# Performance work log

Hardware: AMD Instinct MI355X
Metric: run time of the kernel (lower is better)

Reference implementation:

```python
import jax, jax.numpy as jnp
import numpy as np

BN_EPS = 1e-5


def setup_inputs() -> dict:
    key = jax.random.key(0)
    ks = jax.random.split(key, 5)
    B, T, N, C, O, K, E = 2, 4, 50000, 32, 32, 3, 800000
    x = jax.random.normal(ks[0], (B, T, N, C), dtype=jnp.float32)
    edge_index = jax.random.randint(ks[1], (2, E), 0, N, dtype=jnp.int64)
    edge_weight = jax.random.uniform(ks[2], (E,), dtype=jnp.float32)
    W = jax.random.normal(ks[3], (K, C, O), dtype=jnp.float32) * 0.05
    bias = jnp.zeros((O,), dtype=jnp.float32)
    gamma = jnp.ones((O,), dtype=jnp.float32)
    beta = jnp.zeros((O,), dtype=jnp.float32)
    return {"x": x, "edge_index": edge_index, "edge_weight": edge_weight,
            "W": W, "bias": bias, "gamma": gamma, "beta": beta}


def reference(x, edge_index, edge_weight, W, bias, gamma, beta):
    # x: [B, T, N, C]; edge_index: [2, E]; W: [K, C, O]
    B, T, N, C = x.shape
    K = W.shape[0]
    src, dst = edge_index[0], edge_index[1]

    # Scaled Laplacian L_hat = 2L/lambda_max - I with sym norm, lambda_max=2
    # => L_hat = -D^{-1/2} A D^{-1/2} (zero diagonal), PyG ChebConv default.
    deg = jax.ops.segment_sum(edge_weight, src, num_segments=N)
    safe = jnp.where(deg > 0, deg, 1.0)
    dinv = jnp.where(deg > 0, 1.0 / jnp.sqrt(safe), 0.0)
    norm = -dinv[src] * edge_weight * dinv[dst]  # [E]

    # Batch all (b, t) slices together: [N, M, C] with M = B*T
    xn = jnp.transpose(x, (2, 0, 1, 3)).reshape(N, B * T, C)

    def lap(z):  # sparse SpMM applied to every (b,t) slice at once
        return jax.ops.segment_sum(norm[:, None, None] * z[src], dst,
                                   num_segments=N)

    # Chebyshev recursion: T0 = x, T1 = L_hat x, Tk = 2 L_hat T_{k-1} - T_{k-2}
    Tx_prev2 = xn
    out = jnp.einsum('nmc,co->nmo', Tx_prev2, W[0])
    if K > 1:
        Tx_prev = lap(xn)
        out = out + jnp.einsum('nmc,co->nmo', Tx_prev, W[1])
        for k in range(2, K):
            Tx_k = 2.0 * lap(Tx_prev) - Tx_prev2
            out = out + jnp.einsum('nmc,co->nmo', Tx_k, W[k])
            Tx_prev2, Tx_prev = Tx_prev, Tx_k
    out = out + bias  # [N, M, O]

    # BatchNorm1d in training mode, applied per (b,t) slice over nodes,
    # exactly as the original per-slice loop does (biased variance).
    mean = jnp.mean(out, axis=0, keepdims=True)              # [1, M, O]
    var = jnp.mean((out - mean) ** 2, axis=0, keepdims=True)  # [1, M, O]
    y = gamma * (out - mean) * jax.lax.rsqrt(var + BN_EPS) + beta
    y = jax.nn.relu(y)

    return jnp.transpose(y.reshape(N, B, T, -1), (1, 2, 0, 3))  # [B,T,N,O]
```

## Files before the change

### kernel.cpp

```cpp
#include <hip/hip_runtime.h>

#define NNODES 50000
#define NEDGES 800000
#define MB 8
#define CF 32
#define OF 32
#define FPN 256
#define TOTAL_OUT (MB * NNODES * OF)
#define NREP 8

#define BSH 9
#define BINW 512
#define NB ((NNODES + BINW - 1) / BINW)
#define PH (NB * 2)
#define NBA 512
#define EPB ((NEDGES + NBA - 1) / NBA)
#define CAPL 30
#define LBW 32
#define CH 16
#define BINCAP 14336
#define STCAP 7168
#define WFB ((NNODES / 16 + 3) / 4)
#define DGRID ((NNODES + 1023) / 1024)

typedef unsigned short ushort_t;
typedef unsigned int uint_t;
typedef __attribute__((ext_vector_type(8))) short bf16x8;
typedef __attribute__((ext_vector_type(4))) float f32x4;

__device__ __forceinline__ ushort_t f2bf(float f) {
    uint_t u = __float_as_uint(f);
    u += 0x7FFFu + ((u >> 16) & 1u);
    return (ushort_t)(u >> 16);
}
__device__ __forceinline__ float bflo(uint_t u) { return __uint_as_float(u << 16); }
__device__ __forceinline__ float bfhi(uint_t u) { return __uint_as_float(u & 0xFFFF0000u); }

__device__ __forceinline__ bool detect_is64(const int* ei) {
    int lane = threadIdx.x & 63;
    int v = ei[2 * lane + 1];
    return __ballot(v != 0) == 0ULL;
}

__global__ void __launch_bounds__(256) k_build(const int* __restrict__ ei,
                                               const float* __restrict__ w,
                                               const float* __restrict__ x,
                                               float* __restrict__ deg8,
                                               int* __restrict__ g_cnt,
                                               int* __restrict__ g_realH,
                                               int2* __restrict__ binD,
                                               ushort_t* __restrict__ xn) {
    int blk = blockIdx.x;
    int t = threadIdx.x;
    __shared__ int l_cnt[NB];
    __shared__ int l_base[NB];
    __shared__ ushort_t l_pfx[NB + 1];
    __shared__ int l_half[PH];
    __shared__ int2 l_buf[NB][LBW];
    if (blk < NBA) {
        bool is64 = detect_is64(ei);
        const int2* ei2 = (const int2*)ei;
        for (int i = t; i < NB; i += 256) l_cnt[i] = 0;
        for (int i = t; i < PH; i += 256) l_half[i] = 0;
        __syncthreads();
        int rep = blk & 7;
        int e0 = blk * EPB;
        int e1 = min(e0 + EPB, NEDGES);
        for (int e = e0 + t; e < e1; e += 256) {
            int s, d;
            if (is64) {
                int2 sv = ei2[e];
                int2 dv = ei2[NEDGES + e];
                s = sv.x; d = dv.x;
            } else {
                s = ei[e]; d = ei[NEDGES + e];
            }
            float wt = w[e];
            atomicAdd(&deg8[(size_t)rep * NNODES + s], wt);
            int bin = d >> BSH;
            int half = (d >> 8) & 1;
            int2 entry;
            entry.x = s | ((d & (BINW - 1)) << 16);
            entry.y = __float_as_int(wt);
            int pos = atomicAdd(&l_cnt[bin], 1);
            if (pos < CAPL) {
                l_buf[bin][pos] = entry;
                atomicAdd(&l_half[bin * 2 + half], 1);
            } else {
                int gp = atomicAdd(&g_cnt[bin], 1);
                if (gp < BINCAP) {
                    binD[(size_t)bin * BINCAP + gp] = entry;
                    atomicAdd(&g_realH[bin * 2 + half], 1);
                }
            }
        }
        __syncthreads();
        if (t < NB) {
            int c = min(l_cnt[t], CAPL);
            int p = (c + CH - 1) & ~(CH - 1);
            for (int i = c; i < p; i++) l_buf[t][i] = make_int2(0, 0);
            l_cnt[t] = p;
            if (p > 0) l_base[t] = atomicAdd(&g_cnt[t], p);
        }
        for (int i = t; i < PH; i += 256)
            if (l_half[i] > 0) atomicAdd(&g_realH[i], l_half[i]);
        __syncthreads();
        if (t == 0) {
            int sacc = 0;
            for (int b2 = 0; b2 < NB; b2++) {
                l_pfx[b2] = (ushort_t)sacc;
                sacc += l_cnt[b2];
            }
            l_pfx[NB] = (ushort_t)sacc;
        }
        __syncthreads();
        int total = l_pfx[NB];
        for (int idx = t; idx < total; idx += 256) {
            int lo = 0, hi = NB - 1;
            while (lo < hi) {
                int mid = (lo + hi + 1) >> 1;
                if ((int)l_pfx[mid] <= idx) lo = mid; else hi = mid - 1;
            }
            int rel = idx - (int)l_pfx[lo];
            int gp = l_base[lo] + rel;
            if (gp < BINCAP) binD[(size_t)lo * BINCAP + gp] = l_buf[lo][rel];
        }
    } else {
        int bb = blk - NBA;
        int lane = t & 63;
        int n = bb * 4 + (t >> 6);
        int m = lane >> 3;
        int c = (4 * lane) & 31;
        const float4 v = *(const float4*)(x + ((size_t)m * NNODES + n) * CF + c);
        uint2 d;
        d.x = (uint_t)f2bf(v.x) | ((uint_t)f2bf(v.y) << 16);
        d.y = (uint_t)f2bf(v.z) | ((uint_t)f2bf(v.w) << 16);
        *(uint2*)(xn + (size_t)n * FPN + 4 * lane) = d;
    }
}

__global__ void __launch_bounds__(256) k_pass2(const int* __restrict__ g_cnt,
                                               const int* __restrict__ g_realH,
                                               const int2* __restrict__ binD,
                                               const float* __restrict__ deg8,
                                               int2* __restrict__ csr,
                                               int* __restrict__ csr_off,
                                               float* __restrict__ dinv) {
    __shared__ int2 l_stage[STCAP];
    __shared__ int l_h[256];
    __shared__ int l_ws[4];
    __shared__ int l_red[4];
    __shared__ int l_tot;
    int b = blockIdx.x;
    int t = threadIdx.x;
    if (b >= PH) {
        int n = (b - PH) * 1024 + t;
        #pragma unroll
        for (int i = 0; i < 4; i++, n += 256) {
            if (n < NNODES) {
                float s = 0.0f;
                #pragma unroll
                for (int r = 0; r < NREP; r++) s += deg8[(size_t)r * NNODES + n];
                dinv[n] = (s > 0.0f) ? (1.0f / sqrtf(s)) : 0.0f;
            }
        }
        return;
    }
    int bin = b >> 1, h = b & 1;
    int lane = t & 63, wv = t >> 6;

    int vb = (t < b) ? g_realH[t] : 0;
    #pragma unroll
    for (int off = 32; off >= 1; off >>= 1) vb += __shfl_down(vb, off);
    if (lane == 0) l_red[wv] = vb;
    l_h[t] = 0;
    __syncthreads();
    int base = l_red[0] + l_red[1] + l_red[2] + l_red[3];

    int cnt = min(g_cnt[bin], BINCAP);
    const int2* bp = binD + (size_t)bin * BINCAP;
    for (int i = t; i < cnt; i += 256) {
        int2 e = bp[i];
        int dl = e.x >> 16;
        if (e.y != 0 && (dl >> 8) == h) atomicAdd(&l_h[dl & 255], 1);
    }
    __syncthreads();

    int a0 = l_h[t];
    int v = a0;
    #pragma unroll
    for (int off = 1; off < 64; off <<= 1) {
        int u = __shfl_up(v, off);
        if (lane >= off) v += u;
    }
    if (lane == 63) l_ws[wv] = v;
    __syncthreads();
    int wpre = 0;
    for (int i = 0; i < wv; i++) wpre += l_ws[i];
    int excl = wpre + v - a0;

    int n = bin * BINW + h * 256 + t;
    if (n < NNODES) csr_off[n] = base + excl;
    l_h[t] = excl;
    if (t == 255) {
        l_tot = excl + a0;
        if (b == PH - 1) csr_off[NNODES] = base + excl + a0;
    }
    __syncthreads();

    for (int i = t; i < cnt; i += 256) {
        int2 e = bp[i];
        int dl = e.x >> 16;
        if (e.y != 0 && (dl >> 8) == h) {
            int slot = atomicAdd(&l_h[dl & 255], 1);
            if (slot < STCAP) l_stage[slot] = make_int2(e.x & 0xFFFF, e.y);
        }
    }
    __syncthreads();

    int tot = min(l_tot, STCAP);
    for (int i = t; i < tot; i += 256) csr[(size_t)base + i] = l_stage[i];
}

template <int PHASE>
__global__ void __launch_bounds__(256) k_spmm(const ushort_t* __restrict__ src,
                                              const ushort_t* __restrict__ xn0,
                                              const int* __restrict__ csr_off,
                                              const int2* __restrict__ csr,
                                              const float* __restrict__ dinv,
                                              ushort_t* __restrict__ dst) {
    int t = threadIdx.x;
    int lane = t & 63;
    int n = __builtin_amdgcn_readfirstlane(blockIdx.x * 4 + (t >> 6));
    int off = csr_off[n];
    int cnt = min(csr_off[n + 1] - off, 64);
    float dn = dinv[n];
    float a0 = 0.0f, a1 = 0.0f, a2 = 0.0f, a3 = 0.0f;
    if (cnt > 0) {
        int j = off + min(lane, cnt - 1);
        int2 ed = csr[j];
        int cv = ed.x;
        float vw = -dinv[cv] * __int_as_float(ed.y) * dn;
        uint_t vv = __float_as_uint(vw);
        for (int k = 0; k < cnt; k += 16) {
            int sc[16]; float v[16];
            #pragma unroll
            for (int i = 0; i < 16; i++) {
                sc[i] = __builtin_amdgcn_readlane(cv, k + i);
                float vr = __uint_as_float(__builtin_amdgcn_readlane((int)vv, k + i));
                v[i] = (k + i < cnt) ? vr : 0.0f;
            }
            uint2 u[16];
            #pragma unroll
            for (int i = 0; i < 16; i++)
                u[i] = *(const uint2*)(src + (size_t)sc[i] * FPN + 4 * lane);
            #pragma unroll
            for (int i = 0; i < 16; i++) {
                a0 += v[i] * bflo(u[i].x);
                a1 += v[i] * bfhi(u[i].x);
                a2 += v[i] * bflo(u[i].y);
                a3 += v[i] * bfhi(u[i].y);
            }
        }
    }
    if (PHASE == 2) {
        const uint2 xu = *(const uint2*)(xn0 + (size_t)n * FPN + 4 * lane);
        a0 = 2.0f * a0 - bflo(xu.x);
        a1 = 2.0f * a1 - bfhi(xu.x);
        a2 = 2.0f * a2 - bflo(xu.y);
        a3 = 2.0f * a3 - bfhi(xu.y);
    }
    uint2 d;
    d.x = (uint_t)f2bf(a0) | ((uint_t)f2bf(a1) << 16);
    d.y = (uint_t)f2bf(a2) | ((uint_t)f2bf(a3) << 16);
    *(uint2*)(dst + (size_t)n * FPN + 4 * lane) = d;
}

__global__ void k_wprep(const float* __restrict__ W, ushort_t* __restrict__ wbf) {
    int tid = threadIdx.x;
    for (int i = tid; i < 384; i += 256) {
        int k    = i >> 7;
        int rem  = i & 127;
        int oh   = rem >> 6;
        int lane = rem & 63;
        int quad = lane >> 4;
        int colc = lane & 15;
        ushort_t* d = wbf + (size_t)i * 8;
        for (int j = 0; j < 8; j++) {
            int c = quad * 8 + j;
            int o = oh * 16 + colc;
            d[j] = f2bf(W[k * (CF * OF) + c * OF + o]);
        }
    }
}

__global__ void __launch_bounds__(256) k_wfuse(const ushort_t* __restrict__ xn,
                                               const ushort_t* __restrict__ t1,
                                               const ushort_t* __restrict__ t2,
                                               const ushort_t* __restrict__ wbf,
                                               const float* __restrict__ bias,
                                               float* __restrict__ out) {
    int t = threadIdx.x;
    int lane = t & 63;
    int wv = blockIdx.x * 4 + (t >> 6);
    if (wv >= NNODES / 16) return;
    int n0 = wv * 16;
    int quad = lane >> 4, col = lane & 15;

    bf16x8 B[6];
    #pragma unroll
    for (int i = 0; i < 6; i++)
        B[i] = *(const bf16x8*)(wbf + (size_t)(i * 64 + lane) * 8);
    float blo = bias[col], bhi = bias[16 + col];

    size_t aoff = (size_t)(n0 + col) * FPN + quad * 8;
    #pragma unroll
    for (int m = 0; m < 8; m++) {
        bf16x8 A0 = *(const bf16x8*)(xn + aoff + m * 32);
        bf16x8 A1 = *(const bf16x8*)(t1 + aoff + m * 32);
        bf16x8 A2 = *(const bf16x8*)(t2 + aoff + m * 32);
        f32x4 lo = { blo, blo, blo, blo };
        f32x4 hi = { bhi, bhi, bhi, bhi };
        lo = __builtin_amdgcn_mfma_f32_16x16x32_bf16(A0, B[0], lo, 0, 0, 0);
        hi = __builtin_amdgcn_mfma_f32_16x16x32_bf16(A0, B[1], hi, 0, 0, 0);
        lo = __builtin_amdgcn_mfma_f32_16x16x32_bf16(A1, B[2], lo, 0, 0, 0);
        hi = __builtin_amdgcn_mfma_f32_16x16x32_bf16(A1, B[3], hi, 0, 0, 0);
        lo = __builtin_amdgcn_mfma_f32_16x16x32_bf16(A2, B[4], lo, 0, 0, 0);
        hi = __builtin_amdgcn_mfma_f32_16x16x32_bf16(A2, B[5], hi, 0, 0, 0);
        float* ob = out + ((size_t)m * NNODES + n0 + quad * 4) * OF + col;
        #pragma unroll
        for (int r = 0; r < 4; r++) {
            ob[(size_t)r * OF]      = lo[r];
            ob[(size_t)r * OF + 16] = hi[r];
        }
    }
}

__global__ void __launch_bounds__(256) k_stats(const float* __restrict__ out,
                                               float* __restrict__ stats) {
    int m = blockIdx.y;
    int t = threadIdx.x;
    int o4 = t & 7, row = t >> 3;
    int n0 = blockIdx.x * 1024;
    int nend = min(n0 + 1024, NNODES);
    float sx = 0, sy = 0, sz = 0, sw = 0;
    float qx = 0, qy = 0, qz = 0, qw = 0;
    for (int n = n0 + row; n < nend; n += 32) {
        const float4 v = *(const float4*)(out + ((size_t)m * NNODES + n) * OF + o4 * 4);
        sx += v.x; sy += v.y; sz += v.z; sw += v.w;
        qx += v.x * v.x; qy += v.y * v.y; qz += v.z * v.z; qw += v.w * v.w;
    }
    __shared__ float4 sS[256];
    __shared__ float4 sQ[256];
    sS[t] = make_float4(sx, sy, sz, sw);
    sQ[t] = make_float4(qx, qy, qz, qw);
    __syncthreads();
    for (int off = 16; off >= 1; off >>= 1) {
        if (row < off) {
            float4 a = sS[t], b = sS[t + off * 8];
            sS[t] = make_float4(a.x + b.x, a.y + b.y, a.z + b.z, a.w + b.w);
            float4 c = sQ[t], d = sQ[t + off * 8];
            sQ[t] = make_float4(c.x + d.x, c.y + d.y, c.z + d.z, c.w + d.w);
        }
        __syncthreads();
    }
    if (row == 0) {
        float4 s = sS[t], q = sQ[t];
        int base = m * 32 + o4 * 4;
        atomicAdd(&stats[base + 0], s.x);
        atomicAdd(&stats[base + 1], s.y);
        atomicAdd(&stats[base + 2], s.z);
        atomicAdd(&stats[base + 3], s.w);
        atomicAdd(&stats[256 + base + 0], q.x);
        atomicAdd(&stats[256 + base + 1], q.y);
        atomicAdd(&stats[256 + base + 2], q.z);
        atomicAdd(&stats[256 + base + 3], q.w);
    }
}

__global__ void __launch_bounds__(256) k_final(float* __restrict__ out,
                                               const float* __restrict__ stats,
                                               const float* __restrict__ gamma,
                                               const float* __restrict__ beta) {
    int idx4 = blockIdx.x * 256 + threadIdx.x;
    size_t base = (size_t)idx4 * 4;
    int o = (int)(base & 31);
    int m = (int)(base / ((size_t)NNODES * OF));
    int mo = m * 32 + o;
    const float4 sm = *(const float4*)(stats + mo);
    const float4 sq = *(const float4*)(stats + 256 + mo);
    const float4 g  = *(const float4*)(gamma + o);
    const float4 bt = *(const float4*)(beta + o);
    const float inv_n = 1.0f / (float)NNODES;
    float4 v = *(const float4*)(out + base);
    {
        float mean = sm.x * inv_n, var = sq.x * inv_n - mean * mean;
        float sc = g.x * rsqrtf(var + 1e-5f);
        v.x = fmaxf(v.x * sc + (bt.x - sc * mean), 0.0f);
    }
    {
        float mean = sm.y * inv_n, var = sq.y * inv_n - mean * mean;
        float sc = g.y * rsqrtf(var + 1e-5f);
        v.y = fmaxf(v.y * sc + (bt.y - sc * mean), 0.0f);
    }
    {
        float mean = sm.z * inv_n, var = sq.z * inv_n - mean * mean;
        float sc = g.z * rsqrtf(var + 1e-5f);
        v.z = fmaxf(v.z * sc + (bt.z - sc * mean), 0.0f);
    }
    {
        float mean = sm.w * inv_n, var = sq.w * inv_n - mean * mean;
        float sc = g.w * rsqrtf(var + 1e-5f);
        v.w = fmaxf(v.w * sc + (bt.w - sc * mean), 0.0f);
    }
    *(float4*)(out + base) = v;
}

extern "C" void kernel_launch(void* const* d_in, const int* in_sizes, int n_in,
                              void* d_out, int out_size, void* d_ws, size_t ws_size,
                              hipStream_t stream) {
    const float* x     = (const float*)d_in[0];
    const int*   ei    = (const int*)d_in[1];
    const float* w     = (const float*)d_in[2];
    const float* W     = (const float*)d_in[3];
    const float* bias  = (const float*)d_in[4];
    const float* gamma = (const float*)d_in[5];
    const float* beta  = (const float*)d_in[6];
    float* out = (float*)d_out;

    char* p = (char*)d_ws;
    auto alloc = [&](size_t bytes) {
        char* r = p;
        p += (bytes + 511) & ~(size_t)511;
        return r;
    };
    int*      g_cnt   = (int*)alloc((size_t)NB * 4);
    int*      g_realH = (int*)alloc((size_t)PH * 4);
    float*    stats   = (float*)alloc(512 * 4);
    float*    deg8    = (float*)alloc((size_t)NNODES * NREP * 4);
    float*    dinv    = (float*)alloc((size_t)NNODES * 4);
    int2*     binD    = (int2*)alloc((size_t)NB * BINCAP * 8);
    int2*     csr     = (int2*)alloc((size_t)NEDGES * 8);
    int*      csr_off = (int*)alloc((size_t)(NNODES + 1) * 4);
    ushort_t* wbf     = (ushort_t*)alloc(384 * 8 * 2);
    ushort_t* xn      = (ushort_t*)alloc((size_t)NNODES * FPN * 2);
    ushort_t* t1      = (ushort_t*)alloc((size_t)NNODES * FPN * 2);
    ushort_t* t2      = (ushort_t*)alloc((size_t)NNODES * FPN * 2);

    size_t zlen = (char*)(deg8 + (size_t)NNODES * NREP) - (char*)g_cnt;
    hipMemsetAsync(g_cnt, 0, zlen, stream);

    k_wprep<<<1, 256, 0, stream>>>(W, wbf);
    k_build<<<NBA + NNODES / 4, 256, 0, stream>>>(ei, w, x, deg8, g_cnt, g_realH,
                                                  binD, xn);
    k_pass2<<<PH + DGRID, 256, 0, stream>>>(g_cnt, g_realH, binD, deg8,
                                            csr, csr_off, dinv);

    k_spmm<1><<<NNODES / 4, 256, 0, stream>>>(xn, xn, csr_off, csr, dinv, t1);
    k_spmm<2><<<NNODES / 4, 256, 0, stream>>>(t1, xn, csr_off, csr, dinv, t2);

    k_wfuse<<<WFB, 256, 0, stream>>>(xn, t1, t2, wbf, bias, out);

    dim3 sgrid((NNODES + 1023) / 1024, MB);
    k_stats<<<sgrid, 256, 0, stream>>>(out, stats);
    k_final<<<TOTAL_OUT / 4 / 256, 256, 0, stream>>>(out, stats, gamma, beta);
}
```

Baseline: 357.9 us.

## Precompute normalized edge weights in CSR build and split transpose/dinv kernels

Splits the x transpose and the degree-inverse computation into separate kernels so that dinv is ready before CSR construction. The pass2 kernel then stores the fully normalized edge value (-dinv[src]*w*dinv[dst]) in the CSR, which removes the per-edge dinv gathers from both SpMM passes. It also doubles the number of edge-binning blocks and shrinks the per-block local bin capacity while enlarging the global bin capacity. The cost is two extra kernel launches, plus dinv gathers inside pass2 instead.

Result: slower. 395.7 us (+10.6%).

```diff
diff --git a/kernel.cpp b/kernel.cpp
--- a/kernel.cpp
+++ b/kernel.cpp
@@ -13,15 +13,14 @@
 #define BINW 512
 #define NB ((NNODES + BINW - 1) / BINW)
 #define PH (NB * 2)
-#define NBA 512
+#define NBA 1024
 #define EPB ((NEDGES + NBA - 1) / NBA)
-#define CAPL 30
+#define CAPL 20
 #define LBW 32
 #define CH 16
-#define BINCAP 14336
+#define BINCAP 18432
 #define STCAP 7168
 #define WFB ((NNODES / 16 + 3) / 4)
-#define DGRID ((NNODES + 1023) / 1024)
 
 typedef unsigned short ushort_t;
 typedef unsigned int uint_t;
@@ -42,14 +41,26 @@
     return __ballot(v != 0) == 0ULL;
 }
 
+__global__ void __launch_bounds__(256) k_xpose(const float* __restrict__ x,
+                                               ushort_t* __restrict__ xn) {
+    int t = threadIdx.x;
+    int lane = t & 63;
+    int n = blockIdx.x * 4 + (t >> 6);
+    int m = lane >> 3;
+    int c = (4 * lane) & 31;
+    const float4 v = *(const float4*)(x + ((size_t)m * NNODES + n) * CF + c);
+    uint2 d;
+    d.x = (uint_t)f2bf(v.x) | ((uint_t)f2bf(v.y) << 16);
+    d.y = (uint_t)f2bf(v.z) | ((uint_t)f2bf(v.w) << 16);
+    *(uint2*)(xn + (size_t)n * FPN + 4 * lane) = d;
+}
+
 __global__ void __launch_bounds__(256) k_build(const int* __restrict__ ei,
                                                const float* __restrict__ w,
-                                               const float* __restrict__ x,
                                                float* __restrict__ deg8,
                                                int* __restrict__ g_cnt,
                                                int* __restrict__ g_realH,
-                                               int2* __restrict__ binD,
-                                               ushort_t* __restrict__ xn) {
+                                               int2* __restrict__ binD) {
     int blk = blockIdx.x;
     int t = threadIdx.x;
     __shared__ int l_cnt[NB];
@@ -57,95 +68,91 @@
     __shared__ ushort_t l_pfx[NB + 1];
     __shared__ int l_half[PH];
     __shared__ int2 l_buf[NB][LBW];
-    if (blk < NBA) {
-        bool is64 = detect_is64(ei);
-        const int2* ei2 = (const int2*)ei;
-        for (int i = t; i < NB; i += 256) l_cnt[i] = 0;
-        for (int i = t; i < PH; i += 256) l_half[i] = 0;
-        __syncthreads();
-        int rep = blk & 7;
-        int e0 = blk * EPB;
-        int e1 = min(e0 + EPB, NEDGES);
-        for (int e = e0 + t; e < e1; e += 256) {
-            int s, d;
-            if (is64) {
-                int2 sv = ei2[e];
-                int2 dv = ei2[NEDGES + e];
-                s = sv.x; d = dv.x;
-            } else {
-                s = ei[e]; d = ei[NEDGES + e];
+    bool is64 = detect_is64(ei);
+    const int2* ei2 = (const int2*)ei;
+    for (int i = t; i < NB; i += 256) l_cnt[i] = 0;
+    for (int i = t; i < PH; i += 256) l_half[i] = 0;
+    __syncthreads();
+    int rep = blk & 7;
+    int e0 = blk * EPB;
+    int e1 = min(e0 + EPB, NEDGES);
+    for (int e = e0 + t; e < e1; e += 256) {
+        int s, d;
+        if (is64) {
+            int2 sv = ei2[e];
+            int2 dv = ei2[NEDGES + e];
+            s = sv.x; d = dv.x;
+        } else {
+            s = ei[e]; d = ei[NEDGES + e];
+        }
+        float wt = w[e];
+        atomicAdd(&deg8[(size_t)rep * NNODES + s], wt);
+        int bin = d >> BSH;
+        int half = (d >> 8) & 1;
+        int2 entry;
+        entry.x = s | ((d & (BINW - 1)) << 16);
+        entry.y = __float_as_int(wt);
+        int pos = atomicAdd(&l_cnt[bin], 1);
+        if (pos < CAPL) {
+            l_buf[bin][pos] = entry;
+            atomicAdd(&l_half[bin * 2 + half], 1);
+        } else {
+            int gp = atomicAdd(&g_cnt[bin], 1);
+            if (gp < BINCAP) {
+                binD[(size_t)bin * BINCAP + gp] = entry;
+                atomicAdd(&g_realH[bin * 2 + half], 1);
             }
-            float wt = w[e];
-            atomicAdd(&deg8[(size_t)rep * NNODES + s], wt);
-            int bin = d >> BSH;
-            int half = (d >> 8) & 1;
-            int2 entry;
-            entry.x = s | ((d & (BINW - 1)) << 16);
-            entry.y = __float_as_int(wt);
-            int pos = atomicAdd(&l_cnt[bin], 1);
-            if (pos < CAPL) {
-                l_buf[bin][pos] = entry;
-                atomicAdd(&l_half[bin * 2 + half], 1);
-            } else {
-                int gp = atomicAdd(&g_cnt[bin], 1);
-                if (gp < BINCAP) {
-                    binD[(size_t)bin * BINCAP + gp] = entry;
-                    atomicAdd(&g_realH[bin * 2 + half], 1);
-                }
-            }
-        }
-        __syncthreads();
-        if (t < NB) {
-            int c = min(l_cnt[t], CAPL);
-            int p = (c + CH - 1) & ~(CH - 1);
-            for (int i = c; i < p; i++) l_buf[t][i] = make_int2(0, 0);
-            l_cnt[t] = p;
-            if (p > 0) l_base[t] = atomicAdd(&g_cnt[t], p);
-        }
-        for (int i = t; i < PH; i += 256)
-            if (l_half[i] > 0) atomicAdd(&g_realH[i], l_half[i]);
-        __syncthreads();
-        if (t == 0) {
-            int sacc = 0;
-            for (int b2 = 0; b2 < NB; b2++) {
-                l_pfx[b2] = (ushort_t)sacc;
-                sacc += l_cnt[b2];
-            }
-            l_pfx[NB] = (ushort_t)sacc;
-        }
-        __syncthreads();
-        int total = l_pfx[NB];
-        for (int idx = t; idx < total; idx += 256) {
-            int lo = 0, hi = NB - 1;
-            while (lo < hi) {
-                int mid = (lo + hi + 1) >> 1;
-                if ((int)l_pfx[mid] <= idx) lo = mid; else hi = mid - 1;
-            }
-            int rel = idx - (int)l_pfx[lo];
-            int gp = l_base[lo] + rel;
-            if (gp < BINCAP) binD[(size_t)lo * BINCAP + gp] = l_buf[lo][rel];
-        }
-    } else {
-        int bb = blk - NBA;
-        int lane = t & 63;
-        int n = bb * 4 + (t >> 6);
-        int m = lane >> 3;
-        int c = (4 * lane) & 31;
-        const float4 v = *(const float4*)(x + ((size_t)m * NNODES + n) * CF + c);
-        uint2 d;
-        d.x = (uint_t)f2bf(v.x) | ((uint_t)f2bf(v.y) << 16);
-        d.y = (uint_t)f2bf(v.z) | ((uint_t)f2bf(v.w) << 16);
-        *(uint2*)(xn + (size_t)n * FPN + 4 * lane) = d;
-    }
+        }
+    }
+    __syncthreads();
+    if (t < NB) {
+        int c = min(l_cnt[t], CAPL);
+        int p = (c + CH - 1) & ~(CH - 1);
+        for (int i = c; i < p; i++) l_buf[t][i] = make_int2(0, 0);
+        l_cnt[t] = p;
+        if (p > 0) l_base[t] = atomicAdd(&g_cnt[t], p);
+    }
+    for (int i = t; i < PH; i += 256)
+        if (l_half[i] > 0) atomicAdd(&g_realH[i], l_half[i]);
+    __syncthreads();
+    if (t == 0) {
+        int sacc = 0;
+        for (int b2 = 0; b2 < NB; b2++) {
+            l_pfx[b2] = (ushort_t)sacc;
+            sacc += l_cnt[b2];
+        }
+        l_pfx[NB] = (ushort_t)sacc;
+    }
+    __syncthreads();
+    int total = l_pfx[NB];
+    for (int idx = t; idx < total; idx += 256) {
+        int lo = 0, hi = NB - 1;
+        while (lo < hi) {
+            int mid = (lo + hi + 1) >> 1;
+            if ((int)l_pfx[mid] <= idx) lo = mid; else hi = mid - 1;
+        }
+        int rel = idx - (int)l_pfx[lo];
+        int gp = l_base[lo] + rel;
+        if (gp < BINCAP) binD[(size_t)lo * BINCAP + gp] = l_buf[lo][rel];
+    }
+}
+
+__global__ void __launch_bounds__(256) k_dinv(const float* __restrict__ deg8,
+                                              float* __restrict__ dinv) {
+    int n = blockIdx.x * blockDim.x + threadIdx.x;
+    if (n >= NNODES) return;
+    float s = 0.0f;
+    #pragma unroll
+    for (int r = 0; r < NREP; r++) s += deg8[(size_t)r * NNODES + n];
+    dinv[n] = (s > 0.0f) ? (1.0f / sqrtf(s)) : 0.0f;
 }
 
 __global__ void __launch_bounds__(256) k_pass2(const int* __restrict__ g_cnt,
                                                const int* __restrict__ g_realH,
                                                const int2* __restrict__ binD,
-                                               const float* __restrict__ deg8,
+                                               const float* __restrict__ dinv,
                                                int2* __restrict__ csr,
-                                               int* __restrict__ csr_off,
-                                               float* __restrict__ dinv) {
+                                               int* __restrict__ csr_off) {
     __shared__ int2 l_stage[STCAP];
     __shared__ int l_h[256];
     __shared__ int l_ws[4];
@@ -153,19 +160,6 @@
     __shared__ int l_tot;
     int b = blockIdx.x;
     int t = threadIdx.x;
-    if (b >= PH) {
-        int n = (b - PH) * 1024 + t;
-        #pragma unroll
-        for (int i = 0; i < 4; i++, n += 256) {
-            if (n < NNODES) {
-                float s = 0.0f;
-                #pragma unroll
-                for (int r = 0; r < NREP; r++) s += deg8[(size_t)r * NNODES + n];
-                dinv[n] = (s > 0.0f) ? (1.0f / sqrtf(s)) : 0.0f;
-            }
-        }
-        return;
-    }
     int bin = b >> 1, h = b & 1;
     int lane = t & 63, wv = t >> 6;
 
@@ -212,8 +206,11 @@
         int2 e = bp[i];
         int dl = e.x >> 16;
         if (e.y != 0 && (dl >> 8) == h) {
+            int src = e.x & 0xFFFF;
+            int dst = bin * BINW + dl;
+            float val = -dinv[src] * __int_as_float(e.y) * dinv[dst];
             int slot = atomicAdd(&l_h[dl & 255], 1);
-            if (slot < STCAP) l_stage[slot] = make_int2(e.x & 0xFFFF, e.y);
+            if (slot < STCAP) l_stage[slot] = make_int2(src, __float_as_int(val));
         }
     }
     __syncthreads();
@@ -227,21 +224,18 @@
                                               const ushort_t* __restrict__ xn0,
                                               const int* __restrict__ csr_off,
                                               const int2* __restrict__ csr,
-                                              const float* __restrict__ dinv,
                                               ushort_t* __restrict__ dst) {
     int t = threadIdx.x;
     int lane = t & 63;
     int n = __builtin_amdgcn_readfirstlane(blockIdx.x * 4 + (t >> 6));
     int off = csr_off[n];
     int cnt = min(csr_off[n + 1] - off, 64);
-    float dn = dinv[n];
     float a0 = 0.0f, a1 = 0.0f, a2 = 0.0f, a3 = 0.0f;
     if (cnt > 0) {
         int j = off + min(lane, cnt - 1);
         int2 ed = csr[j];
         int cv = ed.x;
-        float vw = -dinv[cv] * __int_as_float(ed.y) * dn;
-        uint_t vv = __float_as_uint(vw);
+        uint_t vv = (uint_t)ed.y;
         for (int k = 0; k < cnt; k += 16) {
             int sc[16]; float v[16];
             #pragma unroll
@@ -451,13 +445,13 @@
     hipMemsetAsync(g_cnt, 0, zlen, stream);
 
     k_wprep<<<1, 256, 0, stream>>>(W, wbf);
-    k_build<<<NBA + NNODES / 4, 256, 0, stream>>>(ei, w, x, deg8, g_cnt, g_realH,
-                                                  binD, xn);
-    k_pass2<<<PH + DGRID, 256, 0, stream>>>(g_cnt, g_realH, binD, deg8,
-                                            csr, csr_off, dinv);
-
-    k_spmm<1><<<NNODES / 4, 256, 0, stream>>>(xn, xn, csr_off, csr, dinv, t1);
-    k_spmm<2><<<NNODES / 4, 256, 0, stream>>>(t1, xn, csr_off, csr, dinv, t2);
+    k_xpose<<<NNODES / 4, 256, 0, stream>>>(x, xn);
+    k_build<<<NBA, 256, 0, stream>>>(ei, w, deg8, g_cnt, g_realH, binD);
+    k_dinv<<<(NNODES + 255) / 256, 256, 0, stream>>>(deg8, dinv);
+    k_pass2<<<PH, 256, 0, stream>>>(g_cnt, g_realH, binD, dinv, csr, csr_off);
+
+    k_spmm<1><<<NNODES / 4, 256, 0, stream>>>(xn, xn, csr_off, csr, t1);
+    k_spmm<2><<<NNODES / 4, 256, 0, stream>>>(t1, xn, csr_off, csr, t2);
 
     k_wfuse<<<WFB, 256, 0, stream>>>(xn, t1, t2, wbf, bias, out);
 
```
